# Kernel tuning notes

Measured on AMD Instinct MI355X. Metric: run time of the kernel, lower is better.

Reference implementation:

```python
import jax, jax.numpy as jnp
import numpy as np

VOCAB, EMB, HID, T, B = 50257, 512, 1024, 512, 64
R, ALPHA = 8, 16
SCALE = ALPHA / R  # LoRA scaling


def _layer_params(key, in_dim, hid):
    ks = jax.random.split(key, 8)
    stdv = 1.0 / np.sqrt(hid)
    u = lambda k, s: jax.random.uniform(k, s, jnp.float32, -stdv, stdv)
    return dict(
        W_ih=u(ks[0], (4 * hid, in_dim)), b_ih=u(ks[1], (4 * hid,)),
        A_ih=jax.random.normal(ks[2], (R, in_dim)) * 0.01,
        B_ih=jax.random.normal(ks[3], (4 * hid, R)) * 0.01,
        W_hh=u(ks[4], (4 * hid, hid)), b_hh=u(ks[5], (4 * hid,)),
        A_hh=jax.random.normal(ks[6], (R, hid)) * 0.01,
        B_hh=jax.random.normal(ks[7], (4 * hid, R)) * 0.01,
    )


def setup_inputs() -> dict:
    key = jax.random.key(0)
    k_emb, kx, kl, k0, k1 = jax.random.split(key, 5)
    emb = jax.random.normal(k_emb, (VOCAB, EMB), jnp.float32)
    emb = emb.at[0].set(0.0)  # padding_idx=0
    x = jax.random.randint(kx, (B, T), 0, VOCAB)
    lengths = jax.random.randint(kl, (B,), 1, T + 1)
    p0 = _layer_params(k0, EMB, HID)
    p1 = _layer_params(k1, HID, HID)
    inp = {"x": x, "lengths": lengths, "emb": emb}
    for name, p in (("0", p0), ("1", p1)):
        for k, v in p.items():
            inp[f"{k}{name}"] = v
    return inp


def _run_layer(seq, W_ih, b_ih, A_ih, B_ih, W_hh, b_hh, A_hh, B_hh):
    # seq: [T, B, D] -> [T, B, H]; LoRA linear: x@W^T + b + (x@A^T)@B^T * scale
    x_proj = (jnp.einsum('tbd,gd->tbg', seq, W_ih) + b_ih
              + jnp.einsum('tbr,gr->tbg', jnp.einsum('tbd,rd->tbr', seq, A_ih), B_ih) * SCALE)

    def step(carry, xp):
        h, c = carry
        gates = (xp + h @ W_hh.T + b_hh + ((h @ A_hh.T) @ B_hh.T) * SCALE)
        i, f, g, o = jnp.split(gates, 4, axis=-1)
        c = jax.nn.sigmoid(f) * c + jax.nn.sigmoid(i) * jnp.tanh(g)
        h = jax.nn.sigmoid(o) * jnp.tanh(c)
        return (h, c), h

    nb = seq.shape[1]
    hid = W_hh.shape[1]
    h0 = jnp.zeros((nb, hid), seq.dtype)
    _, hs = jax.lax.scan(step, (h0, h0), x_proj)
    return hs


def reference(x, lengths, emb,
              W_ih0, b_ih0, A_ih0, B_ih0, W_hh0, b_hh0, A_hh0, B_hh0,
              W_ih1, b_ih1, A_ih1, B_ih1, W_hh1, b_hh1, A_hh1, B_hh1):
    # embedding lookup (dropout in eval mode = identity)
    h_in = emb[x]                       # [B, T, E]
    h_in = jnp.swapaxes(h_in, 0, 1)     # [T, B, E] for scan
    h_in = _run_layer(h_in, W_ih0, b_ih0, A_ih0, B_ih0, W_hh0, b_hh0, A_hh0, B_hh0)
    h_in = _run_layer(h_in, W_ih1, b_ih1, A_ih1, B_ih1, W_hh1, b_hh1, A_hh1, B_hh1)
    idx = jnp.clip(lengths - 1, 0, None)            # [B]
    last_h = h_in[idx, jnp.arange(h_in.shape[1])]   # [B, H]
    return last_h
```

## Files before the change

### kernel.cpp

```cpp
#include <hip/hip_runtime.h>
#include <stdint.h>

typedef _Float16 f16;
typedef _Float16 f16x8 __attribute__((ext_vector_type(8)));
typedef float f32x4 __attribute__((ext_vector_type(4)));

#define NBATCH 64

__device__ __forceinline__ float sigmoidf_(float x) {
    return 1.0f / (1.0f + __expf(-x));
}
__device__ __forceinline__ float tanh_(float x) {
    x = fminf(fmaxf(x, -15.0f), 15.0f);
    float e = __expf(2.0f * x);
    return (e - 1.0f) / (e + 1.0f);
}

__global__ __launch_bounds__(256) void fold_lora(
    const float* __restrict__ W, const float* __restrict__ Bm,
    const float* __restrict__ Am, f16* __restrict__ dst, int K) {
    int cid = blockIdx.x * 256 + threadIdx.x;
    int kc = K >> 3;
    int r = cid / kc;
    int k0 = (cid - r * kc) * 8;
    float bb[8];
#pragma unroll
    for (int j = 0; j < 8; j++) bb[j] = Bm[r * 8 + j];
#pragma unroll
    for (int i = 0; i < 8; i++) {
        float s = 0.0f;
#pragma unroll
        for (int j = 0; j < 8; j++) s += bb[j] * Am[j * K + k0 + i];
        float v = W[(size_t)r * K + k0 + i] + 2.0f * s;
        dst[(size_t)r * K + k0 + i] = (f16)v;
    }
}

__global__ __launch_bounds__(256) void init_misc(
    const float* __restrict__ bih0, const float* __restrict__ bhh0,
    const float* __restrict__ bih1, const float* __restrict__ bhh1,
    float* __restrict__ bsum0, float* __restrict__ bsum1,
    int* __restrict__ flags0, int* __restrict__ flags1,
    float* __restrict__ c0, float* __restrict__ c1) {
    int i = blockIdx.x * 256 + threadIdx.x;
    if (i < 4096) {
        bsum0[i] = bih0[i] + bhh0[i];
        bsum1[i] = bih1[i] + bhh1[i];
    }
    if (i < 256) { flags0[i] = 0; flags1[i] = 0; }
    c0[i] = 0.0f;
    c1[i] = 0.0f;
}

__global__ __launch_bounds__(256) void embed_gather(
    const int* __restrict__ x, const float* __restrict__ emb,
    f16* __restrict__ seqc, int t0) {
    int lt = blockIdx.x;
    int t = t0 + lt;
#pragma unroll
    for (int c = 0; c < 16; c++) {
        int lin = c * 256 + threadIdx.x;
        int b = lin >> 6;
        int e0 = (lin & 63) * 8;
        int tok = x[b * 512 + t];
        const float* src = emb + (size_t)tok * 512 + e0;
        f16x8 v;
#pragma unroll
        for (int i = 0; i < 8; i++) v[i] = (f16)src[i];
        *(f16x8*)&seqc[((size_t)lt * 64 + b) * 512 + e0] = v;
    }
}

__global__ __launch_bounds__(256) void gemm_nt(
    const f16* __restrict__ A, const f16* __restrict__ Bw,
    float* __restrict__ C, int K, int mtmask, int mtshift) {
    __shared__ f16 As[128 * 40];
    __shared__ f16 Bs[128 * 40];
    int bid = blockIdx.x;
    int mt = bid & mtmask, nt = bid >> mtshift;
    int tid = threadIdx.x;
    int w = tid >> 6, lane = tid & 63;
    int lm = lane & 15, lq = lane >> 4;
    int wm = (w >> 1) * 64, wn = (w & 1) * 64;
    f32x4 acc[4][4];
#pragma unroll
    for (int i = 0; i < 4; i++)
#pragma unroll
        for (int j = 0; j < 4; j++) acc[i][j] = f32x4{0.f, 0.f, 0.f, 0.f};
    const f16* Ab = A + (size_t)mt * 128 * K;
    const f16* Bb = Bw + (size_t)nt * 128 * K;
    int nkc = K >> 5;
    for (int kc = 0; kc < nkc; kc++) {
#pragma unroll
        for (int i = 0; i < 2; i++) {
            int cid = tid + i * 256;
            int r = cid >> 2, c8 = (cid & 3) * 8;
            *(f16x8*)&As[r * 40 + c8] = *(const f16x8*)&Ab[(size_t)r * K + kc * 32 + c8];
            *(f16x8*)&Bs[r * 40 + c8] = *(const f16x8*)&Bb[(size_t)r * K + kc * 32 + c8];
        }
        __syncthreads();
        f16x8 af[4], bf[4];
#pragma unroll
        for (int mi = 0; mi < 4; mi++)
            af[mi] = *(const f16x8*)&As[(wm + mi * 16 + lm) * 40 + lq * 8];
#pragma unroll
        for (int ni = 0; ni < 4; ni++)
            bf[ni] = *(const f16x8*)&Bs[(wn + ni * 16 + lm) * 40 + lq * 8];
#pragma unroll
        for (int mi = 0; mi < 4; mi++)
#pragma unroll
            for (int ni = 0; ni < 4; ni++)
                acc[mi][ni] = __builtin_amdgcn_mfma_f32_16x16x32_f16(
                    af[mi], bf[ni], acc[mi][ni], 0, 0, 0);
        __syncthreads();
    }
#pragma unroll
    for (int mi = 0; mi < 4; mi++)
#pragma unroll
        for (int ni = 0; ni < 4; ni++)
#pragma unroll
            for (int r = 0; r < 4; r++) {
                int m = mt * 128 + wm + mi * 16 + lq * 4 + r;
                int n = nt * 128 + wn + ni * 16 + lm;
                int gate = n >> 10, u = n & 1023;
                C[(size_t)m * 4096 + u * 4 + gate] = acc[mi][ni][r];
            }
}


__device__ __forceinline__ void stage_h(f16* hbuf, const uint32_t* hx, int slot,
                                        int bg, int tid) {
    const uint64_t* hp = (const uint64_t*)hx + (size_t)slot * (NBATCH * 256);
#pragma unroll
    for (int i = 0; i < 16; i++) {
        int lin = tid + i * 256;
        int b = lin >> 8, d = lin & 255;
        uint64_t v = __hip_atomic_load(hp + (size_t)(bg * 16 + b) * 256 + d,
                                       __ATOMIC_RELAXED, __HIP_MEMORY_SCOPE_AGENT);
        *(uint64_t*)((char*)hbuf + (size_t)b * 2064 + (size_t)d * 8) = v;
    }
}

__device__ __forceinline__ f32x4 recur_mfma(const f16* hb, const f16x8* wf) {
    f32x4 a0 = f32x4{0.f, 0.f, 0.f, 0.f};
    f32x4 a1 = f32x4{0.f, 0.f, 0.f, 0.f};
    f32x4 a2 = f32x4{0.f, 0.f, 0.f, 0.f};
    f32x4 a3 = f32x4{0.f, 0.f, 0.f, 0.f};
#pragma unroll
    for (int kk = 0; kk < 32; kk += 4) {
        a0 = __builtin_amdgcn_mfma_f32_16x16x32_f16(*(const f16x8*)(hb + (kk + 0) * 32), wf[kk + 0], a0, 0, 0, 0);
        a1 = __builtin_amdgcn_mfma_f32_16x16x32_f16(*(const f16x8*)(hb + (kk + 1) * 32), wf[kk + 1], a1, 0, 0, 0);
        a2 = __builtin_amdgcn_mfma_f32_16x16x32_f16(*(const f16x8*)(hb + (kk + 2) * 32), wf[kk + 2], a2, 0, 0, 0);
        a3 = __builtin_amdgcn_mfma_f32_16x16x32_f16(*(const f16x8*)(hb + (kk + 3) * 32), wf[kk + 3], a3, 0, 0, 0);
    }
    return (a0 + a1) + (a2 + a3);
}

__device__ __forceinline__ void lstm_phase(
    float* xch, f32x4 pre, const f32x4& xv, const float* bias,
    float& c, int t, int smask, uint32_t* hx, int* flags, int myflag,
    int tid, int g, int lq, int lm, int eb, int eu, int batch, int hidx,
    float* dout, int mylen) {
#pragma unroll
    for (int r = 0; r < 4; r++)
        xch[(g * 16 + lq * 4 + r) * 16 + lm] = pre[r];
    __syncthreads();
    float pg[4];
#pragma unroll
    for (int g2 = 0; g2 < 4; g2++)
        pg[g2] = xch[(g2 * 16 + eb) * 16 + eu] + xv[g2] + bias[g2];
    float iv = sigmoidf_(pg[0]);
    float fv = sigmoidf_(pg[1]);
    float gv = tanh_(pg[2]);
    float ov = sigmoidf_(pg[3]);
    c = fv * c + iv * gv;
    float h = ov * tanh_(c);
    float hn = __shfl_xor(h, 1);
    if ((tid & 1) == 0) {
        f16 a = (f16)h, b2 = (f16)hn;
        uint16_t lo = *(uint16_t*)&a, hi = *(uint16_t*)&b2;
        uint32_t pk = (uint32_t)lo | ((uint32_t)hi << 16);
        __hip_atomic_store(hx + (size_t)(t & smask) * (NBATCH * 512)
                               + (size_t)batch * 512 + (hidx >> 1),
                           pk, __ATOMIC_RELAXED, __HIP_MEMORY_SCOPE_AGENT);
    }
    if (dout != nullptr && t == mylen - 1)
        dout[(size_t)batch * 1024 + hidx] = h;
    __syncthreads();
    if (tid == 0)
        __hip_atomic_store(flags + myflag, t + 1, __ATOMIC_RELAXED,
                           __HIP_MEMORY_SCOPE_AGENT);
}

__global__ __launch_bounds__(256, 1) void lstm_recur2(
    const float* __restrict__ xpA, const f16* __restrict__ WhA,
    const float* __restrict__ bsA, uint32_t* __restrict__ hxA,
    int* __restrict__ flagsA, float* __restrict__ cstA, int t0a, int smaskA,
    const float* __restrict__ xpB, const f16* __restrict__ WhB,
    const float* __restrict__ bsB, uint32_t* __restrict__ hxB,
    int* __restrict__ flagsB, float* __restrict__ cstB, int t0b,
    const int* __restrict__ lengths, float* __restrict__ dout, int nsteps) {
    __shared__ f16 hbufA[16 * 1032];
    __shared__ f16 hbufB[16 * 1032];
    __shared__ float xch[4 * 16 * 16];
    const int tid = threadIdx.x;
    const int g = tid >> 6, lane = tid & 63;
    const int lm = lane & 15, lq = lane >> 4;
    const int bid = blockIdx.x;
    const int bg = bid >> 6, jg = bid & 63;
    const bool hasA = (t0a >= 0), hasB = (t0b >= 0);

    f16x8 wfA[32], wfB[32];
    {
        const int grow = g * 1024 + jg * 16 + lm;
        if (hasA) {
            const f16* wp = WhA + (size_t)grow * 1024 + lq * 8;
#pragma unroll
            for (int kk = 0; kk < 32; kk++) wfA[kk] = *(const f16x8*)(wp + kk * 32);
        }
        if (hasB) {
            const f16* wp = WhB + (size_t)grow * 1024 + lq * 8;
#pragma unroll
            for (int kk = 0; kk < 32; kk++) wfB[kk] = *(const f16x8*)(wp + kk * 32);
        }
    }
    const int eb = tid >> 4, eu = tid & 15;
    const int batch = bg * 16 + eb;
    const int hidx = jg * 16 + eu;
    float biasA[4], biasB[4];
#pragma unroll
    for (int g2 = 0; g2 < 4; g2++) {
        biasA[g2] = hasA ? bsA[g2 * 1024 + hidx] : 0.0f;
        biasB[g2] = hasB ? bsB[g2 * 1024 + hidx] : 0.0f;
    }
    const int mylen = lengths[batch];
    float cA = (hasA && t0a > 0) ? cstA[(size_t)batch * 1024 + hidx] : 0.0f;
    float cB = (hasB && t0b > 0) ? cstB[(size_t)batch * 1024 + hidx] : 0.0f;
    const int myflag = bg * 64 + jg;
    const int* flA = flagsA + bg * 64;
    const int* flB = flagsB + bg * 64;

    for (int lt = 0; lt < nsteps; lt++) {
        const int ta = t0a + lt, tb = t0b + lt;
        const bool doA = hasA && ta > 0;
        const bool doB = hasB && tb > 0;
        f32x4 xvA = f32x4{0.f, 0.f, 0.f, 0.f};
        f32x4 xvB = f32x4{0.f, 0.f, 0.f, 0.f};
        if (hasA)
            xvA = *(const f32x4*)(xpA + ((size_t)lt * 64 + batch) * 4096 + (hidx << 2));
        if (hasB)
            xvB = *(const f32x4*)(xpB + ((size_t)lt * 64 + batch) * 4096 + (hidx << 2));
        if (tid < 64) {
            if (doA) {
                for (;;) {
                    int v = __hip_atomic_load(flA + tid, __ATOMIC_RELAXED,
                                              __HIP_MEMORY_SCOPE_AGENT);
                    if (__all(v >= ta)) break;
                    __builtin_amdgcn_s_sleep(1);
                }
            }
            if (doB) {
                for (;;) {
                    int v = __hip_atomic_load(flB + tid, __ATOMIC_RELAXED,
                                              __HIP_MEMORY_SCOPE_AGENT);
                    if (__all(v >= tb)) break;
                    __builtin_amdgcn_s_sleep(1);
                }
            }
        }
        __syncthreads();
        if (doA) stage_h(hbufA, hxA, (ta - 1) & smaskA, bg, tid);
        if (doB) stage_h(hbufB, hxB, (tb - 1) & 1, bg, tid);
        __syncthreads();

        if (hasA) {
            f32x4 pre = f32x4{0.f, 0.f, 0.f, 0.f};
            if (doA) pre = recur_mfma(&hbufA[lm * 1032 + lq * 8], wfA);
            lstm_phase(xch, pre, xvA, biasA, cA, ta, smaskA, hxA, flagsA, myflag,
                       tid, g, lq, lm, eb, eu, batch, hidx, nullptr, -1);
        }
        if (hasB) {
            f32x4 pre = f32x4{0.f, 0.f, 0.f, 0.f};
            if (doB) pre = recur_mfma(&hbufB[lm * 1032 + lq * 8], wfB);
            lstm_phase(xch, pre, xvB, biasB, cB, tb, 1, hxB, flagsB, myflag,
                       tid, g, lq, lm, eb, eu, batch, hidx, dout, mylen);
        }
    }
    if (hasA) cstA[(size_t)batch * 1024 + hidx] = cA;
    if (hasB) cstB[(size_t)batch * 1024 + hidx] = cB;
}

extern "C" void kernel_launch(void* const* d_in, const int* in_sizes, int n_in,
                              void* d_out, int out_size, void* d_ws, size_t ws_size,
                              hipStream_t stream) {
    const int*   x     = (const int*)d_in[0];
    const int*   len   = (const int*)d_in[1];
    const float* emb   = (const float*)d_in[2];
    const float* W_ih0 = (const float*)d_in[3];
    const float* b_ih0 = (const float*)d_in[4];
    const float* A_ih0 = (const float*)d_in[5];
    const float* B_ih0 = (const float*)d_in[6];
    const float* W_hh0 = (const float*)d_in[7];
    const float* b_hh0 = (const float*)d_in[8];
    const float* A_hh0 = (const float*)d_in[9];
    const float* B_hh0 = (const float*)d_in[10];
    const float* W_ih1 = (const float*)d_in[11];
    const float* b_ih1 = (const float*)d_in[12];
    const float* A_ih1 = (const float*)d_in[13];
    const float* B_ih1 = (const float*)d_in[14];
    const float* W_hh1 = (const float*)d_in[15];
    const float* b_hh1 = (const float*)d_in[16];
    const float* A_hh1 = (const float*)d_in[17];
    const float* B_hh1 = (const float*)d_in[18];

    char* ws = (char*)d_ws;
    size_t off = 0;
    auto alloc = [&](size_t bytes) {
        size_t o = off;
        off += (bytes + 255) & ~(size_t)255;
        return o;
    };
    f16*   W0f    = (f16*)(ws + alloc((size_t)4096 * 512 * 2));
    f16*   Wh0f   = (f16*)(ws + alloc((size_t)4096 * 1024 * 2));
    f16*   W1f    = (f16*)(ws + alloc((size_t)4096 * 1024 * 2));
    f16*   Wh1f   = (f16*)(ws + alloc((size_t)4096 * 1024 * 2));
    float* bsum0  = (float*)(ws + alloc(4096 * 4));
    float* bsum1  = (float*)(ws + alloc(4096 * 4));
    int*   flags0 = (int*)(ws + alloc(4096));
    int*   flags1 = (int*)(ws + alloc(4096));
    float* c0st   = (float*)(ws + alloc((size_t)64 * 1024 * 4));
    float* c1st   = (float*)(ws + alloc((size_t)64 * 1024 * 4));
    f16*   hx1    = (f16*)(ws + alloc((size_t)2 * 64 * 1024 * 2));

    int CHv = 64;
    {
        auto al = [](size_t b) { return (b + 255) & ~(size_t)255; };
        size_t need = off
            + al((size_t)64 * 64 * 512 * 2)
            + al((size_t)64 * 64 * 1024 * 2)
            + 2 * al((size_t)64 * 64 * 4096 * 4);
        if (ws_size < need) CHv = 32;
    }
    const int NCHv = 512 / CHv;
    f16*   seqc = (f16*)(ws + alloc((size_t)CHv * 64 * 512 * 2));
    f16*   h0c  = (f16*)(ws + alloc((size_t)CHv * 64 * 1024 * 2));
    float* xp0c = (float*)(ws + alloc((size_t)CHv * 64 * 4096 * 4));
    float* xp1c = (float*)(ws + alloc((size_t)CHv * 64 * 4096 * 4));
    const int mtiles  = (CHv * 64) / 128;
    const int mtmask  = mtiles - 1;
    const int mtshift = (CHv == 64) ? 5 : 4;
    (void)in_sizes; (void)n_in; (void)out_size;

    fold_lora<<<1024, 256, 0, stream>>>(W_ih0, B_ih0, A_ih0, W0f, 512);
    fold_lora<<<2048, 256, 0, stream>>>(W_hh0, B_hh0, A_hh0, Wh0f, 1024);
    fold_lora<<<2048, 256, 0, stream>>>(W_ih1, B_ih1, A_ih1, W1f, 1024);
    fold_lora<<<2048, 256, 0, stream>>>(W_hh1, B_hh1, A_hh1, Wh1f, 1024);
    init_misc<<<256, 256, 0, stream>>>(b_ih0, b_hh0, b_ih1, b_hh1,
                                       bsum0, bsum1, flags0, flags1, c0st, c1st);

    for (int c = 0; c <= NCHv; c++) {
        if (c < NCHv) {
            embed_gather<<<CHv, 256, 0, stream>>>(x, emb, seqc, c * CHv);
            gemm_nt<<<mtiles * 32, 256, 0, stream>>>(seqc, W0f, xp0c, 512,
                                                     mtmask, mtshift);
        }
        if (c > 0)
            gemm_nt<<<mtiles * 32, 256, 0, stream>>>(h0c, W1f, xp1c, 1024,
                                                     mtmask, mtshift);
        lstm_recur2<<<256, 256, 0, stream>>>(
            xp0c, Wh0f, bsum0, (uint32_t*)h0c, flags0, c0st,
            (c < NCHv) ? c * CHv : -1, CHv - 1,
            xp1c, Wh1f, bsum1, (uint32_t*)hx1, flags1, c1st,
            (c > 0) ? (c - 1) * CHv : -1,
            len, (float*)d_out, CHv);
    }
}
```

Measured before the change: 7.405 ms.

## Merge per-layer step flags into one shared flag and trim barriers

The two interleaved LSTM layers now share one per-step flag counter, so each block does a single spin-wait and publishes a single flag per step instead of one per layer. The inlined phase code swaps __syncthreads for a barrier that waits only on LDS counters, and the per-layer trailing barriers collapse into one before the flag store. This cuts cross-block polling and barrier overhead on the serial critical path. The risks are memory ordering, since the global h stores are no longer waited on before the barrier, and the flag base needing to stay consistent across launches.

Result: slower. 7.696 ms (+3.9%).

```diff
diff --git a/kernel.cpp b/kernel.cpp
--- a/kernel.cpp
+++ b/kernel.cpp
@@ -14,6 +14,12 @@
     x = fminf(fmaxf(x, -15.0f), 15.0f);
     float e = __expf(2.0f * x);
     return (e - 1.0f) / (e + 1.0f);
+}
+
+__device__ __forceinline__ void lds_barrier() {
+    asm volatile("s_waitcnt lgkmcnt(0)" ::: "memory");
+    __builtin_amdgcn_s_barrier();
+    asm volatile("" ::: "memory");
 }
 
 __global__ __launch_bounds__(256) void fold_lora(
@@ -156,49 +162,14 @@
     return (a0 + a1) + (a2 + a3);
 }
 
-__device__ __forceinline__ void lstm_phase(
-    float* xch, f32x4 pre, const f32x4& xv, const float* bias,
-    float& c, int t, int smask, uint32_t* hx, int* flags, int myflag,
-    int tid, int g, int lq, int lm, int eb, int eu, int batch, int hidx,
-    float* dout, int mylen) {
-#pragma unroll
-    for (int r = 0; r < 4; r++)
-        xch[(g * 16 + lq * 4 + r) * 16 + lm] = pre[r];
-    __syncthreads();
-    float pg[4];
-#pragma unroll
-    for (int g2 = 0; g2 < 4; g2++)
-        pg[g2] = xch[(g2 * 16 + eb) * 16 + eu] + xv[g2] + bias[g2];
-    float iv = sigmoidf_(pg[0]);
-    float fv = sigmoidf_(pg[1]);
-    float gv = tanh_(pg[2]);
-    float ov = sigmoidf_(pg[3]);
-    c = fv * c + iv * gv;
-    float h = ov * tanh_(c);
-    float hn = __shfl_xor(h, 1);
-    if ((tid & 1) == 0) {
-        f16 a = (f16)h, b2 = (f16)hn;
-        uint16_t lo = *(uint16_t*)&a, hi = *(uint16_t*)&b2;
-        uint32_t pk = (uint32_t)lo | ((uint32_t)hi << 16);
-        __hip_atomic_store(hx + (size_t)(t & smask) * (NBATCH * 512)
-                               + (size_t)batch * 512 + (hidx >> 1),
-                           pk, __ATOMIC_RELAXED, __HIP_MEMORY_SCOPE_AGENT);
-    }
-    if (dout != nullptr && t == mylen - 1)
-        dout[(size_t)batch * 1024 + hidx] = h;
-    __syncthreads();
-    if (tid == 0)
-        __hip_atomic_store(flags + myflag, t + 1, __ATOMIC_RELAXED,
-                           __HIP_MEMORY_SCOPE_AGENT);
-}
-
 __global__ __launch_bounds__(256, 1) void lstm_recur2(
     const float* __restrict__ xpA, const f16* __restrict__ WhA,
     const float* __restrict__ bsA, uint32_t* __restrict__ hxA,
-    int* __restrict__ flagsA, float* __restrict__ cstA, int t0a, int smaskA,
+    float* __restrict__ cstA, int t0a, int smaskA,
     const float* __restrict__ xpB, const f16* __restrict__ WhB,
     const float* __restrict__ bsB, uint32_t* __restrict__ hxB,
-    int* __restrict__ flagsB, float* __restrict__ cstB, int t0b,
+    float* __restrict__ cstB, int t0b,
+    int* __restrict__ flags, int fbase,
     const int* __restrict__ lengths, float* __restrict__ dout, int nsteps) {
     __shared__ f16 hbufA[16 * 1032];
     __shared__ f16 hbufB[16 * 1032];
@@ -237,8 +208,7 @@
     float cA = (hasA && t0a > 0) ? cstA[(size_t)batch * 1024 + hidx] : 0.0f;
     float cB = (hasB && t0b > 0) ? cstB[(size_t)batch * 1024 + hidx] : 0.0f;
     const int myflag = bg * 64 + jg;
-    const int* flA = flagsA + bg * 64;
-    const int* flB = flagsB + bg * 64;
+    const int* fl = flags + bg * 64;
 
     for (int lt = 0; lt < nsteps; lt++) {
         const int ta = t0a + lt, tb = t0b + lt;
@@ -251,21 +221,11 @@
         if (hasB)
             xvB = *(const f32x4*)(xpB + ((size_t)lt * 64 + batch) * 4096 + (hidx << 2));
         if (tid < 64) {
-            if (doA) {
-                for (;;) {
-                    int v = __hip_atomic_load(flA + tid, __ATOMIC_RELAXED,
-                                              __HIP_MEMORY_SCOPE_AGENT);
-                    if (__all(v >= ta)) break;
-                    __builtin_amdgcn_s_sleep(1);
-                }
-            }
-            if (doB) {
-                for (;;) {
-                    int v = __hip_atomic_load(flB + tid, __ATOMIC_RELAXED,
-                                              __HIP_MEMORY_SCOPE_AGENT);
-                    if (__all(v >= tb)) break;
-                    __builtin_amdgcn_s_sleep(1);
-                }
+            for (;;) {
+                int v = __hip_atomic_load(fl + tid, __ATOMIC_RELAXED,
+                                          __HIP_MEMORY_SCOPE_AGENT);
+                if (__all(v >= fbase + lt)) break;
+                __builtin_amdgcn_s_sleep(1);
             }
         }
         __syncthreads();
@@ -276,15 +236,56 @@
         if (hasA) {
             f32x4 pre = f32x4{0.f, 0.f, 0.f, 0.f};
             if (doA) pre = recur_mfma(&hbufA[lm * 1032 + lq * 8], wfA);
-            lstm_phase(xch, pre, xvA, biasA, cA, ta, smaskA, hxA, flagsA, myflag,
-                       tid, g, lq, lm, eb, eu, batch, hidx, nullptr, -1);
+#pragma unroll
+            for (int r = 0; r < 4; r++)
+                xch[(g * 16 + lq * 4 + r) * 16 + lm] = pre[r];
+            lds_barrier();
+            float pg[4];
+#pragma unroll
+            for (int g2 = 0; g2 < 4; g2++)
+                pg[g2] = xch[(g2 * 16 + eb) * 16 + eu] + xvA[g2] + biasA[g2];
+            cA = sigmoidf_(pg[1]) * cA + sigmoidf_(pg[0]) * tanh_(pg[2]);
+            float h = sigmoidf_(pg[3]) * tanh_(cA);
+            float hn = __shfl_xor(h, 1);
+            if ((tid & 1) == 0) {
+                f16 a = (f16)h, b2 = (f16)hn;
+                uint16_t lo = *(uint16_t*)&a, hi = *(uint16_t*)&b2;
+                uint32_t pk = (uint32_t)lo | ((uint32_t)hi << 16);
+                __hip_atomic_store(hxA + (size_t)(ta & smaskA) * (NBATCH * 512)
+                                       + (size_t)batch * 512 + (hidx >> 1),
+                                   pk, __ATOMIC_RELAXED, __HIP_MEMORY_SCOPE_AGENT);
+            }
+            lds_barrier();
         }
         if (hasB) {
             f32x4 pre = f32x4{0.f, 0.f, 0.f, 0.f};
             if (doB) pre = recur_mfma(&hbufB[lm * 1032 + lq * 8], wfB);
-            lstm_phase(xch, pre, xvB, biasB, cB, tb, 1, hxB, flagsB, myflag,
-                       tid, g, lq, lm, eb, eu, batch, hidx, dout, mylen);
-        }
+#pragma unroll
+            for (int r = 0; r < 4; r++)
+                xch[(g * 16 + lq * 4 + r) * 16 + lm] = pre[r];
+            lds_barrier();
+            float pg[4];
+#pragma unroll
+            for (int g2 = 0; g2 < 4; g2++)
+                pg[g2] = xch[(g2 * 16 + eb) * 16 + eu] + xvB[g2] + biasB[g2];
+            cB = sigmoidf_(pg[1]) * cB + sigmoidf_(pg[0]) * tanh_(pg[2]);
+            float h = sigmoidf_(pg[3]) * tanh_(cB);
+            float hn = __shfl_xor(h, 1);
+            if ((tid & 1) == 0) {
+                f16 a = (f16)h, b2 = (f16)hn;
+                uint16_t lo = *(uint16_t*)&a, hi = *(uint16_t*)&b2;
+                uint32_t pk = (uint32_t)lo | ((uint32_t)hi << 16);
+                __hip_atomic_store(hxB + (size_t)(tb & 1) * (NBATCH * 512)
+                                       + (size_t)batch * 512 + (hidx >> 1),
+                                   pk, __ATOMIC_RELAXED, __HIP_MEMORY_SCOPE_AGENT);
+            }
+            if (dout != nullptr && tb == mylen - 1)
+                dout[(size_t)batch * 1024 + hidx] = h;
+        }
+        __syncthreads();
+        if (tid == 0)
+            __hip_atomic_store(flags + myflag, fbase + lt + 1, __ATOMIC_RELAXED,
+                               __HIP_MEMORY_SCOPE_AGENT);
     }
     if (hasA) cstA[(size_t)batch * 1024 + hidx] = cA;
     if (hasB) cstB[(size_t)batch * 1024 + hidx] = cB;
@@ -368,10 +369,11 @@
             gemm_nt<<<mtiles * 32, 256, 0, stream>>>(h0c, W1f, xp1c, 1024,
                                                      mtmask, mtshift);
         lstm_recur2<<<256, 256, 0, stream>>>(
-            xp0c, Wh0f, bsum0, (uint32_t*)h0c, flags0, c0st,
+            xp0c, Wh0f, bsum0, (uint32_t*)h0c, c0st,
             (c < NCHv) ? c * CHv : -1, CHv - 1,
-            xp1c, Wh1f, bsum1, (uint32_t*)hx1, flags1, c1st,
+            xp1c, Wh1f, bsum1, (uint32_t*)hx1, c1st,
             (c > 0) ? (c - 1) * CHv : -1,
+            flags0, c * CHv,
             len, (float*)d_out, CHv);
     }
 }
```

## Run the two LSTM layer recurrences in separate co-resident blocks

Applied to the files above, without the earlier changes.

Before, each of the 256 blocks ran both layer chains back to back inside every timestep, sharing barriers and flag waits, so the two layers were serialized per step. Now a 512-block grid gives each layer its own 256 blocks, each with a single weight-fragment set and one shared-memory h buffer, so two blocks share a CU. The two layers can then progress independently and overlap their sync and matrix latency. In exchange it relies on all 512 blocks being co-resident for the spin-wait flags, and the two blocks on a CU compete for registers and matrix throughput.

After: 6.009 ms. -18.9%, faster.

```diff
diff --git a/kernel.cpp b/kernel.cpp
--- a/kernel.cpp
+++ b/kernel.cpp
@@ -156,43 +156,92 @@
     return (a0 + a1) + (a2 + a3);
 }
 
-__device__ __forceinline__ void lstm_phase(
-    float* xch, f32x4 pre, const f32x4& xv, const float* bias,
-    float& c, int t, int smask, uint32_t* hx, int* flags, int myflag,
-    int tid, int g, int lq, int lm, int eb, int eu, int batch, int hidx,
-    float* dout, int mylen) {
-#pragma unroll
-    for (int r = 0; r < 4; r++)
-        xch[(g * 16 + lq * 4 + r) * 16 + lm] = pre[r];
-    __syncthreads();
-    float pg[4];
-#pragma unroll
-    for (int g2 = 0; g2 < 4; g2++)
-        pg[g2] = xch[(g2 * 16 + eb) * 16 + eu] + xv[g2] + bias[g2];
-    float iv = sigmoidf_(pg[0]);
-    float fv = sigmoidf_(pg[1]);
-    float gv = tanh_(pg[2]);
-    float ov = sigmoidf_(pg[3]);
-    c = fv * c + iv * gv;
-    float h = ov * tanh_(c);
-    float hn = __shfl_xor(h, 1);
-    if ((tid & 1) == 0) {
-        f16 a = (f16)h, b2 = (f16)hn;
-        uint16_t lo = *(uint16_t*)&a, hi = *(uint16_t*)&b2;
-        uint32_t pk = (uint32_t)lo | ((uint32_t)hi << 16);
-        __hip_atomic_store(hx + (size_t)(t & smask) * (NBATCH * 512)
-                               + (size_t)batch * 512 + (hidx >> 1),
-                           pk, __ATOMIC_RELAXED, __HIP_MEMORY_SCOPE_AGENT);
-    }
-    if (dout != nullptr && t == mylen - 1)
-        dout[(size_t)batch * 1024 + hidx] = h;
-    __syncthreads();
-    if (tid == 0)
-        __hip_atomic_store(flags + myflag, t + 1, __ATOMIC_RELAXED,
-                           __HIP_MEMORY_SCOPE_AGENT);
-}
-
-__global__ __launch_bounds__(256, 1) void lstm_recur2(
+__device__ __forceinline__ void chain_loop(
+    const float* __restrict__ xp, const f16* __restrict__ Wh,
+    const float* __restrict__ bsum, uint32_t* __restrict__ hexch,
+    int* __restrict__ flags, float* __restrict__ cstate,
+    int t0, int smask, const int* __restrict__ lengths,
+    float* __restrict__ dout, int bid, int nsteps,
+    f16* hbuf, float* xch) {
+    int tid = threadIdx.x;
+    int g = tid >> 6, lane = tid & 63;
+    int lm = lane & 15, lq = lane >> 4;
+    int bg = bid >> 6, jg = bid & 63;
+
+    f16x8 wfrag[32];
+    {
+        int grow = g * 1024 + jg * 16 + lm;
+        const f16* wp = Wh + (size_t)grow * 1024 + lq * 8;
+#pragma unroll
+        for (int kk = 0; kk < 32; kk++) wfrag[kk] = *(const f16x8*)(wp + kk * 32);
+    }
+    int eb = tid >> 4, eu = tid & 15;
+    int batch = bg * 16 + eb;
+    int hidx = jg * 16 + eu;
+    float bias[4];
+#pragma unroll
+    for (int g2 = 0; g2 < 4; g2++) bias[g2] = bsum[g2 * 1024 + hidx];
+    int mylen = (lengths != nullptr) ? lengths[batch] : -1;
+    float c = (t0 > 0) ? cstate[(size_t)batch * 1024 + hidx] : 0.0f;
+    const int myflag = bg * 64 + jg;
+
+    for (int lt = 0; lt < nsteps; lt++) {
+        int t = t0 + lt;
+        const f32x4 xpv = *(const f32x4*)(xp + ((size_t)lt * 64 + batch) * 4096 + (hidx << 2));
+        f32x4 pre = f32x4{0.f, 0.f, 0.f, 0.f};
+        if (t > 0) {
+            if (tid < 64) {
+                const int* fl = flags + bg * 64;
+                for (;;) {
+                    int v = __hip_atomic_load(fl + tid, __ATOMIC_RELAXED,
+                                              __HIP_MEMORY_SCOPE_AGENT);
+                    if (__all(v >= t)) break;
+                    __builtin_amdgcn_s_sleep(1);
+                }
+            }
+            __syncthreads();
+            stage_h(hbuf, hexch, (t - 1) & smask, bg, tid);
+            __syncthreads();
+            pre = recur_mfma(&hbuf[lm * 1032 + lq * 8], wfrag);
+        }
+#pragma unroll
+        for (int r = 0; r < 4; r++)
+            xch[(g * 16 + lq * 4 + r) * 16 + lm] = pre[r];
+        __syncthreads();
+        float pg[4];
+#pragma unroll
+        for (int g2 = 0; g2 < 4; g2++)
+            pg[g2] = xch[(g2 * 16 + eb) * 16 + eu] + xpv[g2] + bias[g2];
+        float iv = sigmoidf_(pg[0]);
+        float fv = sigmoidf_(pg[1]);
+        float gv = tanh_(pg[2]);
+        float ov = sigmoidf_(pg[3]);
+        c = fv * c + iv * gv;
+        float h = ov * tanh_(c);
+        float hn = __shfl_xor(h, 1);
+        if ((tid & 1) == 0) {
+            uint16_t lo, hi;
+            {
+                f16 a = (f16)h, b2 = (f16)hn;
+                lo = *(uint16_t*)&a; hi = *(uint16_t*)&b2;
+            }
+            uint32_t pk = (uint32_t)lo | ((uint32_t)hi << 16);
+            __hip_atomic_store(
+                hexch + (size_t)(t & smask) * (NBATCH * 512)
+                      + (size_t)batch * 512 + (hidx >> 1),
+                pk, __ATOMIC_RELAXED, __HIP_MEMORY_SCOPE_AGENT);
+        }
+        if (dout != nullptr && t == mylen - 1)
+            dout[(size_t)batch * 1024 + hidx] = h;
+        __syncthreads();
+        if (tid == 0)
+            __hip_atomic_store(flags + myflag, t + 1, __ATOMIC_RELAXED,
+                               __HIP_MEMORY_SCOPE_AGENT);
+    }
+    cstate[(size_t)batch * 1024 + hidx] = c;
+}
+
+__global__ __launch_bounds__(256, 2) void lstm_dual(
     const float* __restrict__ xpA, const f16* __restrict__ WhA,
     const float* __restrict__ bsA, uint32_t* __restrict__ hxA,
     int* __restrict__ flagsA, float* __restrict__ cstA, int t0a, int smaskA,
@@ -200,94 +249,18 @@
     const float* __restrict__ bsB, uint32_t* __restrict__ hxB,
     int* __restrict__ flagsB, float* __restrict__ cstB, int t0b,
     const int* __restrict__ lengths, float* __restrict__ dout, int nsteps) {
-    __shared__ f16 hbufA[16 * 1032];
-    __shared__ f16 hbufB[16 * 1032];
+    __shared__ f16 hbuf[16 * 1032];
     __shared__ float xch[4 * 16 * 16];
-    const int tid = threadIdx.x;
-    const int g = tid >> 6, lane = tid & 63;
-    const int lm = lane & 15, lq = lane >> 4;
-    const int bid = blockIdx.x;
-    const int bg = bid >> 6, jg = bid & 63;
-    const bool hasA = (t0a >= 0), hasB = (t0b >= 0);
-
-    f16x8 wfA[32], wfB[32];
-    {
-        const int grow = g * 1024 + jg * 16 + lm;
-        if (hasA) {
-            const f16* wp = WhA + (size_t)grow * 1024 + lq * 8;
-#pragma unroll
-            for (int kk = 0; kk < 32; kk++) wfA[kk] = *(const f16x8*)(wp + kk * 32);
-        }
-        if (hasB) {
-            const f16* wp = WhB + (size_t)grow * 1024 + lq * 8;
-#pragma unroll
-            for (int kk = 0; kk < 32; kk++) wfB[kk] = *(const f16x8*)(wp + kk * 32);
-        }
-    }
-    const int eb = tid >> 4, eu = tid & 15;
-    const int batch = bg * 16 + eb;
-    const int hidx = jg * 16 + eu;
-    float biasA[4], biasB[4];
-#pragma unroll
-    for (int g2 = 0; g2 < 4; g2++) {
-        biasA[g2] = hasA ? bsA[g2 * 1024 + hidx] : 0.0f;
-        biasB[g2] = hasB ? bsB[g2 * 1024 + hidx] : 0.0f;
-    }
-    const int mylen = lengths[batch];
-    float cA = (hasA && t0a > 0) ? cstA[(size_t)batch * 1024 + hidx] : 0.0f;
-    float cB = (hasB && t0b > 0) ? cstB[(size_t)batch * 1024 + hidx] : 0.0f;
-    const int myflag = bg * 64 + jg;
-    const int* flA = flagsA + bg * 64;
-    const int* flB = flagsB + bg * 64;
-
-    for (int lt = 0; lt < nsteps; lt++) {
-        const int ta = t0a + lt, tb = t0b + lt;
-        const bool doA = hasA && ta > 0;
-        const bool doB = hasB && tb > 0;
-        f32x4 xvA = f32x4{0.f, 0.f, 0.f, 0.f};
-        f32x4 xvB = f32x4{0.f, 0.f, 0.f, 0.f};
-        if (hasA)
-            xvA = *(const f32x4*)(xpA + ((size_t)lt * 64 + batch) * 4096 + (hidx << 2));
-        if (hasB)
-            xvB = *(const f32x4*)(xpB + ((size_t)lt * 64 + batch) * 4096 + (hidx << 2));
-        if (tid < 64) {
-            if (doA) {
-                for (;;) {
-                    int v = __hip_atomic_load(flA + tid, __ATOMIC_RELAXED,
-                                              __HIP_MEMORY_SCOPE_AGENT);
-                    if (__all(v >= ta)) break;
-                    __builtin_amdgcn_s_sleep(1);
-                }
-            }
-            if (doB) {
-                for (;;) {
-                    int v = __hip_atomic_load(flB + tid, __ATOMIC_RELAXED,
-                                              __HIP_MEMORY_SCOPE_AGENT);
-                    if (__all(v >= tb)) break;
-                    __builtin_amdgcn_s_sleep(1);
-                }
-            }
-        }
-        __syncthreads();
-        if (doA) stage_h(hbufA, hxA, (ta - 1) & smaskA, bg, tid);
-        if (doB) stage_h(hbufB, hxB, (tb - 1) & 1, bg, tid);
-        __syncthreads();
-
-        if (hasA) {
-            f32x4 pre = f32x4{0.f, 0.f, 0.f, 0.f};
-            if (doA) pre = recur_mfma(&hbufA[lm * 1032 + lq * 8], wfA);
-            lstm_phase(xch, pre, xvA, biasA, cA, ta, smaskA, hxA, flagsA, myflag,
-                       tid, g, lq, lm, eb, eu, batch, hidx, nullptr, -1);
-        }
-        if (hasB) {
-            f32x4 pre = f32x4{0.f, 0.f, 0.f, 0.f};
-            if (doB) pre = recur_mfma(&hbufB[lm * 1032 + lq * 8], wfB);
-            lstm_phase(xch, pre, xvB, biasB, cB, tb, 1, hxB, flagsB, myflag,
-                       tid, g, lq, lm, eb, eu, batch, hidx, dout, mylen);
-        }
-    }
-    if (hasA) cstA[(size_t)batch * 1024 + hidx] = cA;
-    if (hasB) cstB[(size_t)batch * 1024 + hidx] = cB;
+    const int cid = blockIdx.x;
+    if (cid < 256) {
+        if (t0a < 0) return;
+        chain_loop(xpA, WhA, bsA, hxA, flagsA, cstA, t0a, smaskA,
+                   nullptr, nullptr, cid, nsteps, hbuf, xch);
+    } else {
+        if (t0b < 0) return;
+        chain_loop(xpB, WhB, bsB, hxB, flagsB, cstB, t0b, 1,
+                   lengths, dout, cid - 256, nsteps, hbuf, xch);
+    }
 }
 
 extern "C" void kernel_launch(void* const* d_in, const int* in_sizes, int n_in,
@@ -367,7 +340,7 @@
         if (c > 0)
             gemm_nt<<<mtiles * 32, 256, 0, stream>>>(h0c, W1f, xp1c, 1024,
                                                      mtmask, mtshift);
-        lstm_recur2<<<256, 256, 0, stream>>>(
+        lstm_dual<<<512, 256, 0, stream>>>(
             xp0c, Wh0f, bsum0, (uint32_t*)h0c, flags0, c0st,
             (c < NCHv) ? c * CHv : -1, CHv - 1,
             xp1c, Wh1f, bsum1, (uint32_t*)hx1, flags1, c1st,
```
